# Kernel tuning notes

Hardware: AMD Instinct MI355X
Metric: run time of the kernel (lower is better)

## Reference

```python
import jax, jax.numpy as jnp
import numpy as np

V, E, H = 32000, 1024, 1024  # vocab, wemb, enc
T1, B = 129, 64


def setup_inputs() -> dict:
    key = jax.random.key(0)
    ks = jax.random.split(key, 6)
    sH = 1.0 / np.sqrt(H)
    data = jax.random.randint(ks[0], (T1, B), 0, V)
    mask = jnp.ones((T1, B), jnp.float32)
    emb = jax.random.normal(ks[1], (V, E), jnp.float32) * 0.02
    W_ih = jax.random.normal(ks[2], (E, 4 * H), jnp.float32) * sH
    W_hh = jax.random.normal(ks[3], (H, 4 * H), jnp.float32) * sH
    b = jnp.zeros((4 * H,), jnp.float32)
    Wr = jax.random.normal(ks[4], (E, H), jnp.float32) * sH  # readout: Linear(H -> E), torch weight (out,in)
    br = jnp.zeros((E,), jnp.float32)
    bd = jnp.zeros((V,), jnp.float32)  # decoder bias (weight tied to emb)
    return {"data": data, "mask": mask, "emb": emb, "W_ih": W_ih, "W_hh": W_hh,
            "b": b, "Wr": Wr, "br": br, "bd": bd}


def reference(data, mask, emb, W_ih, W_hh, b, Wr, br, bd):
    x_data = data[:-1]          # [Tx, B]
    y_data = data[1:]           # [Tx, B]
    m_all = mask[1:]            # note: source uses mask[1:] for BOTH x_mask and y_mask
    Tx, Bn = x_data.shape

    def step(carry, xs):
        ht, ct, loss = carry
        tx, ty, mt = xs                      # [B], [B], [B]
        x = emb[tx]                          # [B, E] embedding lookup
        g = x @ W_ih + ht @ W_hh + b         # [B, 4H]
        i, f, gg, o = jnp.split(g, 4, axis=1)
        i = jax.nn.sigmoid(i); f = jax.nn.sigmoid(f); o = jax.nn.sigmoid(o)
        gg = jnp.tanh(gg)
        cn = f * ct + i * gg
        hn = o * jnp.tanh(cn)
        mm = mt[:, None]
        ht2 = mm * hn + (1.0 - mm) * ht      # masked state update
        ct2 = mm * cn + (1.0 - mm) * ct
        out = ht2 @ Wr.T + br                # readout [B, E]
        logit = out @ emb.T + bd             # tied decoder [B, V]
        logp = jax.nn.log_softmax(logit, axis=1)
        nll = -jnp.take_along_axis(logp, ty[:, None], axis=1)[:, 0]
        loss = loss + jnp.mean(nll * mt)     # loss_reduction == 'org'
        return (ht2, ct2, loss), None

    init = (jnp.zeros((Bn, H), jnp.float32), jnp.zeros((Bn, H), jnp.float32),
            jnp.zeros((), jnp.float32))
    (_, _, loss), _ = jax.lax.scan(step, init, (x_data, y_data, m_all))
    return loss / Bn
```

## Files before the change

kernel.cpp:

```cpp
#include <hip/hip_runtime.h>
#include <stdint.h>

#define V_  32000
#define E_  1024
#define H_  1024
#define B_  64
#define T_  128
#define MROWS (T_ * B_)
#define NCB_ 250
#define NTG  32
#define ITEMS_PER_TG 258
#define TOTAL_ITEMS (NTG * ITEMS_PER_TG)

typedef __bf16 bf16x8 __attribute__((ext_vector_type(8)));
typedef float  f32x4  __attribute__((ext_vector_type(4)));

__device__ __forceinline__ uint16_t f2b(float f) {
  uint32_t u = __builtin_bit_cast(uint32_t, f);
  return (uint16_t)((u + 0x7fffu + ((u >> 16) & 1u)) >> 16);
}
__device__ __forceinline__ float b2f(uint16_t h) {
  uint32_t u = ((uint32_t)h) << 16;
  return __builtin_bit_cast(float, u);
}
__device__ __forceinline__ float fsig_(float x) {
  return __builtin_amdgcn_rcpf(1.0f + __expf(-x));
}
__device__ __forceinline__ float ftanh_(float x) {
  return 2.0f * __builtin_amdgcn_rcpf(1.0f + __expf(-2.0f * x)) - 1.0f;
}

__device__ __forceinline__ void gload16(const uint16_t* g, uint16_t* l) {
  __builtin_amdgcn_global_load_lds(
      (const __attribute__((address_space(1))) uint32_t*)g,
      (__attribute__((address_space(3))) uint32_t*)l,
      16, 0, 0);
}


__global__ void k_cvt(const float* __restrict__ src, uint16_t* __restrict__ dst, int n4) {
  int i = blockIdx.x * blockDim.x + threadIdx.x;
  int st = gridDim.x * blockDim.x;
  for (; i < n4; i += st) {
    float4 v = ((const float4*)src)[i];
    ushort4 o;
    o.x = f2b(v.x); o.y = f2b(v.y); o.z = f2b(v.z); o.w = f2b(v.w);
    ((ushort4*)dst)[i] = o;
  }
}

__global__ void k_tcvt(const float* __restrict__ src, uint16_t* __restrict__ dst,
                       int R, int C, int dstStride, int dstOff) {
  __shared__ float tile[32][33];
  int c0 = blockIdx.x * 32, r0 = blockIdx.y * 32;
  int tx = threadIdx.x, ty = threadIdx.y;
  for (int j = 0; j < 32; j += 8)
    tile[ty + j][tx] = src[(size_t)(r0 + ty + j) * C + c0 + tx];
  __syncthreads();
  for (int j = 0; j < 32; j += 8)
    dst[(size_t)(c0 + ty + j) * dstStride + dstOff + r0 + tx] = f2b(tile[tx][ty + j]);
}

__global__ void k_zero(uint4* p, int n) {
  int i = blockIdx.x * blockDim.x + threadIdx.x;
  int st = gridDim.x * blockDim.x;
  uint4 z = {0, 0, 0, 0};
  for (; i < n; i += st) p[i] = z;
}

__global__ __launch_bounds__(256) void k_xw(
    const int* __restrict__ data, const uint16_t* __restrict__ embB,
    const uint16_t* __restrict__ Wcat,
    const float* __restrict__ bias, uint16_t* __restrict__ xAll)
{
  __shared__ uint16_t lA[128 * 64];
  __shared__ uint16_t lB[128 * 64];

  int tid = threadIdx.x;
  int w = tid >> 6, l = tid & 63, lr = l & 15, lg = l >> 4;
  int wr = w >> 1, wc = w & 1;
  int m0 = blockIdx.x * 128;
  int n0 = blockIdx.y * 128;

  int stRow = l >> 3;
  int kswz  = ((l & 7) * 8) ^ ((stRow & 7) << 3);
  const uint16_t* aSrc[4];
  const uint16_t* bSrc[4];
#pragma unroll
  for (int cc = 0; cc < 4; ++cc) {
    int tok = data[m0 + w * 32 + cc * 8 + stRow];
    aSrc[cc] = embB + (size_t)tok * 1024 + kswz;
    bSrc[cc] = Wcat + (size_t)(n0 + w * 32 + cc * 8 + stRow) * 2048 + kswz;
  }

  f32x4 acc[4][4] = {};

  for (int kt = 0; kt < 1024; kt += 64) {
#pragma unroll
    for (int cc = 0; cc < 4; ++cc) {
      gload16(aSrc[cc] + kt, &lA[(w * 4 + cc) * 512]);
      gload16(bSrc[cc] + kt, &lB[(w * 4 + cc) * 512]);
    }
    __syncthreads();
#pragma unroll
    for (int ksub = 0; ksub < 2; ++ksub) {
      bf16x8 af[4], bfr[4];
      int ke = ksub * 32 + lg * 8;
#pragma unroll
      for (int mi = 0; mi < 4; ++mi) {
        int row = wr * 64 + mi * 16 + lr;
        af[mi] = *(const bf16x8*)&lA[row * 64 + (ke ^ ((row & 7) << 3))];
      }
#pragma unroll
      for (int ni = 0; ni < 4; ++ni) {
        int row = wc * 64 + ni * 16 + lr;
        bfr[ni] = *(const bf16x8*)&lB[row * 64 + (ke ^ ((row & 7) << 3))];
      }
#pragma unroll
      for (int mi = 0; mi < 4; ++mi)
#pragma unroll
        for (int ni = 0; ni < 4; ++ni)
          acc[mi][ni] = __builtin_amdgcn_mfma_f32_16x16x32_bf16(af[mi], bfr[ni], acc[mi][ni], 0, 0, 0);
    }
    __syncthreads();
  }

  float bv[4];
#pragma unroll
  for (int ni = 0; ni < 4; ++ni) bv[ni] = bias[n0 + wc * 64 + ni * 16 + lr];
#pragma unroll
  for (int mi = 0; mi < 4; ++mi)
#pragma unroll
    for (int ni = 0; ni < 4; ++ni) {
      int row = wr * 64 + mi * 16 + lg * 4;
      int col = n0 + wc * 64 + ni * 16 + lr;
#pragma unroll
      for (int r = 0; r < 4; ++r)
        xAll[(size_t)(m0 + row + r) * 4096 + col] = f2b(acc[mi][ni][r] + bv[ni]);
    }
}

__global__ __launch_bounds__(512) void k_mega(
    const uint16_t* __restrict__ xAll, const uint16_t* __restrict__ Wcat,
    const float* __restrict__ mask, uint16_t* __restrict__ hAll,
    uint32_t* __restrict__ flags,
    const uint16_t* __restrict__ embB, const uint16_t* __restrict__ WrB,
    const float* __restrict__ br, const float* __restrict__ bd,
    uint16_t* __restrict__ outAll, float2* __restrict__ part,
    uint32_t* __restrict__ projDone, uint32_t* __restrict__ workCtr)
{
  __shared__ alignas(16) char smem[151552];

  int tid = threadIdx.x;
  int blk = blockIdx.x;
  int w = tid >> 6, l = tid & 63, lr = l & 15, lg = l >> 4;

  if (blk < 64) {
    uint16_t* wh    = (uint16_t*)smem;
    uint16_t* xs0   = (uint16_t*)(smem + 131072);
    uint16_t* xs1   = (uint16_t*)(smem + 139264);
    uint16_t* hp0   = (uint16_t*)(smem + 147456);
    uint16_t* hp1   = (uint16_t*)(smem + 149504);
    uint16_t* xsb[2] = {xs0, xs1};
    uint16_t* hpb[2] = {hp0, hp1};

    int u0 = blk * 16;

    for (int it = 0; it < 16; ++it) {
      int ch = it * 512 + tid;
      int c  = ch >> 7;
      int kb = (ch & 127) * 16;
      int gRow = (c & 3) * 1024 + u0 + (c >> 2);
      uint4 v = *(const uint4*)((const char*)Wcat + (size_t)gRow * 4096 + 2048 + kb);
      *(uint4*)((char*)wh + c * 2048 + (kb ^ ((c & 7) << 4))) = v;
    }

    int wm = w >> 1, wn = w & 1;
    int q = lr & 3;

    const char* wb0 = (const char*)wh + (size_t)(wn * 32 + lr) * 2048;
    const char* wb1 = (const char*)wh + (size_t)(wn * 32 + 16 + lr) * 2048;
    int xr = (lr & 7) << 4;

    int sRow = tid >> 3, sQ = (tid >> 1) & 3, sHalf = tid & 1;
    const uint16_t* xSrc = xAll + (size_t)sRow * 4096 + sQ * 1024 + u0 + sHalf * 8;
    int xDstOff = sRow * 64 + sQ * 16 + sHalf * 8;
    int xoBase = (wm * 16 + lg * 4) * 64 + q * 16 + wn * 8 + (lr >> 2);

    float cR[2][4] = {}, hR[2][4] = {};

    *(uint4*)&xsb[0][xDstOff] = *(const uint4*)xSrc;
    __syncthreads();

    int cur = 0;
    for (int t = 0; t < T_; ++t) {
      float xwv[2][4], mm_[4];
#pragma unroll
      for (int ni = 0; ni < 2; ++ni)
#pragma unroll
        for (int r = 0; r < 4; ++r)
          xwv[ni][r] = b2f(xsb[cur][xoBase + r * 64 + ni * 4]);
#pragma unroll
      for (int r = 0; r < 4; ++r)
        mm_[r] = mask[(t + 1) * B_ + wm * 16 + lg * 4 + r];

      if (t + 1 < T_)
        *(uint4*)&xsb[cur ^ 1][xDstOff] = *(const uint4*)(xSrc + (size_t)(t + 1) * B_ * 4096);

      if (t > 0) {
        uint32_t tv = (uint32_t)t;
        while (!__all((int)(__hip_atomic_load(&flags[l], __ATOMIC_RELAXED,
                                              __HIP_MEMORY_SCOPE_AGENT) >= tv)))
          __builtin_amdgcn_s_sleep(1);
        asm volatile("" ::: "memory");
      }

      const uint16_t* aH = hAll + (size_t)t * (B_ * H_) + (size_t)(wm * 16 + lr) * H_ + lg * 8;

      f32x4 acc0 = {0.f, 0.f, 0.f, 0.f}, acc1 = {0.f, 0.f, 0.f, 0.f};
#pragma unroll 8
      for (int ks = 0; ks < 32; ++ks) {
        bf16x8 a = *(const bf16x8*)(aH + ks * 32);
        int ko = (ks * 64 + lg * 16) ^ xr;
        bf16x8 b0 = *(const bf16x8*)(wb0 + ko);
        bf16x8 b1 = *(const bf16x8*)(wb1 + ko);
        acc0 = __builtin_amdgcn_mfma_f32_16x16x32_bf16(a, b0, acc0, 0, 0, 0);
        acc1 = __builtin_amdgcn_mfma_f32_16x16x32_bf16(a, b1, acc1, 0, 0, 0);
      }

#pragma unroll
      for (int ni = 0; ni < 2; ++ni) {
        f32x4 accv = ni ? acc1 : acc0;
#pragma unroll
        for (int r = 0; r < 4; ++r) {
          float v0 = accv[r] + xwv[ni][r];
          float v1 = __shfl_xor(v0, 1, 64);
          float v2 = __shfl_xor(v0, 2, 64);
          float v3 = __shfl_xor(v0, 3, 64);
          float gi = (q == 0) ? v0 : (q == 1) ? v1 : (q == 2) ? v2 : v3;
          float gf = (q == 1) ? v0 : (q == 0) ? v1 : (q == 3) ? v2 : v3;
          float gg = (q == 2) ? v0 : (q == 3) ? v1 : (q == 0) ? v2 : v3;
          float go = (q == 3) ? v0 : (q == 2) ? v1 : (q == 1) ? v2 : v3;
          gi = fsig_(gi); gf = fsig_(gf); gg = ftanh_(gg); go = fsig_(go);
          float cn = gf * cR[ni][r] + gi * gg;
          float hn = go * ftanh_(cn);
          float mm = mm_[r];
          cR[ni][r] = mm * cn + (1.f - mm) * cR[ni][r];
          hR[ni][r] = mm * hn + (1.f - mm) * hR[ni][r];
          if (q == 0)
            hpb[cur][(wm * 16 + lg * 4 + r) * 16 + wn * 8 + ni * 4 + (lr >> 2)] = f2b(hR[ni][r]);
        }
      }

      __syncthreads();

      if (w == 0) {
        const unsigned long long* hp = (const unsigned long long*)hpb[cur];
        unsigned long long* hd =
            (unsigned long long*)(hAll + (size_t)(t + 1) * (B_ * H_) + (size_t)l * H_ + u0);
#pragma unroll
        for (int j = 0; j < 4; ++j)
          __hip_atomic_store(hd + j, hp[l * 4 + j],
                             __ATOMIC_RELAXED, __HIP_MEMORY_SCOPE_AGENT);
        asm volatile("s_waitcnt vmcnt(0)" ::: "memory");
        if (l == 0)
          __hip_atomic_store(&flags[blk], (uint32_t)(t + 1),
                             __ATOMIC_RELAXED, __HIP_MEMORY_SCOPE_AGENT);
      }
      cur ^= 1;
    }
  } else {
    uint16_t* lA  = (uint16_t*)smem;
    uint16_t* lB  = (uint16_t*)(smem + 32768);
    float2*   cm  = (float2*)(smem + 49152);
    uint32_t* sId = (uint32_t*)(smem + 53248);

    int stRow = l >> 3;
    int kswz  = ((l & 7) * 8) ^ ((stRow & 7) << 3);
    int wr = w >> 1;
    int wc = w & 1;

    for (;;) {
      __syncthreads();
      if (tid == 0)
        *sId = __hip_atomic_fetch_add(workCtr, 1u, __ATOMIC_RELAXED, __HIP_MEMORY_SCOPE_AGENT);
      __syncthreads();
      uint32_t id = *sId;
      if (id >= TOTAL_ITEMS) break;
      int tg = (int)(id / ITEMS_PER_TG), sub = (int)(id % ITEMS_PER_TG);
      int t0 = tg * 4;
      bool isProj = (sub < 8);

      const uint16_t* Abase;
      const uint16_t* Bbase;
      const float* biasp;
      if (isProj) {
        uint32_t tv = (uint32_t)(t0 + 4);
        while (!__all((int)(__hip_atomic_load(&flags[l], __ATOMIC_RELAXED,
                                              __HIP_MEMORY_SCOPE_AGENT) >= tv)))
          __builtin_amdgcn_s_sleep(4);
        asm volatile("" ::: "memory");
        Abase = hAll + (size_t)(t0 + 1) * (B_ * H_);
        Bbase = WrB + (size_t)(sub * 128) * 1024;
        biasp = br + sub * 128;
      } else {
        while (__hip_atomic_load(&projDone[tg], __ATOMIC_RELAXED,
                                 __HIP_MEMORY_SCOPE_AGENT) < 8u)
          __builtin_amdgcn_s_sleep(4);
        asm volatile("" ::: "memory");
        Abase = outAll + (size_t)t0 * B_ * 1024;
        Bbase = embB + (size_t)(sub - 8) * 128 * 1024;
        biasp = bd + (sub - 8) * 128;
      }

      const uint16_t* aS = Abase + (size_t)(w * 32 + stRow) * 1024 + kswz;
      const uint16_t* bS = Bbase + (size_t)(w * 16 + stRow) * 1024 + kswz;

      f32x4 acc[4][4] = {};
      for (int kt = 0; kt < 1024; kt += 64) {
#pragma unroll
        for (int cc = 0; cc < 4; ++cc)
          gload16(aS + (size_t)cc * 8 * 1024 + kt, &lA[(w * 4 + cc) * 512]);
#pragma unroll
        for (int cc = 0; cc < 2; ++cc)
          gload16(bS + (size_t)cc * 8 * 1024 + kt, &lB[(w * 2 + cc) * 512]);
        __syncthreads();
#pragma unroll
        for (int ksub = 0; ksub < 2; ++ksub) {
          int ke = ksub * 32 + lg * 8;
          bf16x8 af[4], bfr[4];
#pragma unroll
          for (int mi = 0; mi < 4; ++mi) {
            int row = wr * 64 + mi * 16 + lr;
            af[mi] = *(const bf16x8*)&lA[row * 64 + (ke ^ ((row & 7) << 3))];
          }
#pragma unroll
          for (int ni = 0; ni < 4; ++ni) {
            int row = wc * 64 + ni * 16 + lr;
            bfr[ni] = *(const bf16x8*)&lB[row * 64 + (ke ^ ((row & 7) << 3))];
          }
#pragma unroll
          for (int mi = 0; mi < 4; ++mi)
#pragma unroll
            for (int ni = 0; ni < 4; ++ni)
              acc[mi][ni] = __builtin_amdgcn_mfma_f32_16x16x32_bf16(af[mi], bfr[ni], acc[mi][ni], 0, 0, 0);
        }
        __syncthreads();
      }

      float bv[4];
#pragma unroll
      for (int ni = 0; ni < 4; ++ni) bv[ni] = biasp[wc * 64 + ni * 16 + lr];

      if (isProj) {
        int e0 = sub * 128;
        uint16_t* opack = lA;
#pragma unroll
        for (int chunk = 0; chunk < 4; ++chunk) {
          if (wr == chunk) {
#pragma unroll
            for (int mi = 0; mi < 4; ++mi)
#pragma unroll
              for (int ni = 0; ni < 4; ++ni)
#pragma unroll
                for (int r = 0; r < 4; ++r)
                  opack[(mi * 16 + lg * 4 + r) * 128 + wc * 64 + ni * 16 + lr]
                    = f2b(acc[mi][ni][r] + bv[ni]);
          }
          __syncthreads();
          const unsigned long long* op = (const unsigned long long*)opack;
#pragma unroll
          for (int j = 0; j < 4; ++j) {
            int g = j * 512 + tid;
            int row = g >> 5, seg = g & 31;
            unsigned long long* od =
                (unsigned long long*)(outAll + ((size_t)(t0 + chunk) * B_ + row) * 1024 + e0) + seg;
            __hip_atomic_store(od, op[g], __ATOMIC_RELAXED, __HIP_MEMORY_SCOPE_AGENT);
          }
          __syncthreads();
        }
        asm volatile("s_waitcnt vmcnt(0)" ::: "memory");
        __syncthreads();
        if (tid == 0)
          __hip_atomic_fetch_add(&projDone[tg], 1u, __ATOMIC_RELAXED, __HIP_MEMORY_SCOPE_AGENT);
      } else {
        int nc = sub - 8;
#pragma unroll
        for (int mi = 0; mi < 4; ++mi) {
#pragma unroll
          for (int r = 0; r < 4; ++r) {
            float mx = -1e30f;
#pragma unroll
            for (int ni = 0; ni < 4; ++ni) { acc[mi][ni][r] += bv[ni]; mx = fmaxf(mx, acc[mi][ni][r]); }
#pragma unroll
            for (int d = 1; d < 16; d <<= 1) mx = fmaxf(mx, __shfl_xor(mx, d, 64));
            float s = 0.f;
#pragma unroll
            for (int ni = 0; ni < 4; ++ni) s += expf(acc[mi][ni][r] - mx);
#pragma unroll
            for (int d = 1; d < 16; d <<= 1) s += __shfl_xor(s, d, 64);
            if (lr == 0) cm[wc * 256 + wr * 64 + mi * 16 + lg * 4 + r] = make_float2(mx, s);
          }
        }
        __syncthreads();
        if (tid < 256) {
          float2 p0 = cm[tid], p1 = cm[256 + tid];
          float M = fmaxf(p0.x, p1.x);
          float S = p0.y * expf(p0.x - M) + p1.y * expf(p1.x - M);
          part[(size_t)nc * MROWS + (size_t)t0 * B_ + tid] = make_float2(M, S);
        }
      }
    }
  }
}

__global__ __launch_bounds__(256) void k_tgt(
    const uint16_t* __restrict__ outAll, const uint16_t* __restrict__ embB,
    const float* __restrict__ bd, const int* __restrict__ data, float* __restrict__ tgt)
{
  int w = threadIdx.x >> 6, l = threadIdx.x & 63;
  int row = blockIdx.x * 4 + w;
  int t = row >> 6, b = row & 63;
  int ty = data[(t + 1) * B_ + b];
  const uint16_t* a = outAll + (size_t)row * E_;
  const uint16_t* e = embB + (size_t)ty * E_;
  float s = 0.f;
#pragma unroll
  for (int i0 = 0; i0 < 2; ++i0) {
    int i = (l + i0 * 64) * 8;
    bf16x8 av = *(const bf16x8*)(a + i);
    bf16x8 ev = *(const bf16x8*)(e + i);
#pragma unroll
    for (int j = 0; j < 8; ++j) s += (float)av[j] * (float)ev[j];
  }
#pragma unroll
  for (int d = 1; d < 64; d <<= 1) s += __shfl_xor(s, d, 64);
  if (l == 0) tgt[row] = s + bd[ty];
}

__global__ __launch_bounds__(256) void k_lse(
    const float2* __restrict__ part, const float* __restrict__ tgt,
    const float* __restrict__ mask, float* __restrict__ rowNll)
{
  int w = threadIdx.x >> 6, l = threadIdx.x & 63;
  int row = blockIdx.x * 4 + w;
  float m = -1e30f, s = 0.f;
  for (int cc = l; cc < NCB_; cc += 64) {
    float2 v = part[(size_t)cc * MROWS + row];
    float M = fmaxf(m, v.x);
    s = s * expf(m - M) + v.y * expf(v.x - M);
    m = M;
  }
#pragma unroll
  for (int d = 1; d < 64; d <<= 1) {
    float om = __shfl_xor(m, d, 64);
    float os = __shfl_xor(s, d, 64);
    float M = fmaxf(m, om);
    s = s * expf(m - M) + os * expf(om - M);
    m = M;
  }
  if (l == 0) {
    int t = row >> 6, b = row & 63;
    float nll = (m + logf(s)) - tgt[row];
    rowNll[row] = nll * mask[(t + 1) * B_ + b];
  }
}

__global__ void k_final2(const float* __restrict__ rowNll, float* __restrict__ out) {
  __shared__ float red[256];
  float s = 0.f;
  for (int i = threadIdx.x; i < MROWS; i += 256) s += rowNll[i];
  red[threadIdx.x] = s;
  __syncthreads();
  for (int st = 128; st > 0; st >>= 1) {
    if ((int)threadIdx.x < st) red[threadIdx.x] += red[threadIdx.x + st];
    __syncthreads();
  }
  if (threadIdx.x == 0) out[0] = red[0] / (float)(B_ * B_);
}

extern "C" void kernel_launch(void* const* d_in, const int* in_sizes, int n_in,
                              void* d_out, int out_size, void* d_ws, size_t ws_size,
                              hipStream_t stream)
{
  const int*   data = (const int*)  d_in[0];
  const float* mask = (const float*)d_in[1];
  const float* emb  = (const float*)d_in[2];
  const float* W_ih = (const float*)d_in[3];
  const float* W_hh = (const float*)d_in[4];
  const float* bias = (const float*)d_in[5];
  const float* Wr   = (const float*)d_in[6];
  const float* br   = (const float*)d_in[7];
  const float* bd   = (const float*)d_in[8];
  (void)in_sizes; (void)n_in; (void)out_size; (void)ws_size;

  char* ws = (char*)d_ws;
  size_t off = 0;
  auto alloc = [&](size_t bytes) -> char* {
    char* p = ws + off;
    off += (bytes + 255) & ~(size_t)255;
    return p;
  };
  uint16_t* embB   = (uint16_t*)alloc((size_t)V_ * E_ * 2);
  uint16_t* Wcat   = (uint16_t*)alloc((size_t)4 * H_ * 2048 * 2);
  uint16_t* WrB    = (uint16_t*)alloc((size_t)E_ * H_ * 2);
  uint16_t* hAll   = (uint16_t*)alloc((size_t)(T_ + 1) * B_ * H_ * 2);
  uint16_t* xAll   = (uint16_t*)alloc((size_t)MROWS * 4096 * 2);
  uint16_t* outAll = (uint16_t*)alloc((size_t)MROWS * E_ * 2);
  float2*   part   = (float2*)  alloc((size_t)NCB_ * MROWS * 8);
  float*    tgt    = (float*)   alloc((size_t)MROWS * 4);
  float*    rowNll = (float*)   alloc((size_t)MROWS * 4);
  uint32_t* syncb  = (uint32_t*)alloc(4096);
  uint32_t* flags    = syncb;
  uint32_t* projDone = syncb + 128;
  uint32_t* workCtr  = syncb + 512;

  k_cvt <<<2048, 256, 0, stream>>>(emb, embB, V_ * E_ / 4);
  k_cvt <<<256,  256, 0, stream>>>(Wr, WrB, E_ * H_ / 4);
  k_tcvt<<<dim3(4 * H_ / 32, E_ / 32), dim3(32, 8), 0, stream>>>(W_ih, Wcat, E_, 4 * H_, 2048, 0);
  k_tcvt<<<dim3(4 * H_ / 32, H_ / 32), dim3(32, 8), 0, stream>>>(W_hh, Wcat, H_, 4 * H_, 2048, 1024);
  k_zero<<<32, 256, 0, stream>>>((uint4*)hAll, B_ * H_ * 2 / 16);
  k_zero<<<1, 256, 0, stream>>>((uint4*)syncb, 4096 / 16);

  k_xw<<<dim3(MROWS / 128, 4096 / 128), 256, 0, stream>>>(data, embB, Wcat, bias, xAll);

  k_mega<<<256, 512, 0, stream>>>(xAll, Wcat, mask, hAll, flags,
                                  embB, WrB, br, bd, outAll, part,
                                  projDone, workCtr);

  k_tgt   <<<MROWS / 4, 256, 0, stream>>>(outAll, embB, bd, data, tgt);
  k_lse   <<<MROWS / 4, 256, 0, stream>>>(part, tgt, mask, rowNll);
  k_final2<<<1, 256, 0, stream>>>(rowNll, (float*)d_out);
}
```

Before: 2.128 ms.

## Split recurrent step wait into per-chunk flag waits and prefetch x-projection two steps ahead

The recurrent LSTM loop no longer waits for every producer flag before starting the h@W_hh matmul. It ballots the flags and waits only for the 16-lane group covering each K chunk, processing chunks in a block-rotated order so the MFMAs on ready chunks overlap with waiting on the rest. The x-projection input is now prefetched into a register two steps ahead instead of being loaded synchronously one step ahead. Consumer-side spin sleeps in the projection/decoder workers are lengthened to reduce polling pressure. The risk is extra ballot overhead and loop control on the critical serial path.

```diff
diff --git a/kernel.cpp b/kernel.cpp
--- a/kernel.cpp
+++ b/kernel.cpp
@@ -186,14 +186,20 @@
     const uint16_t* xSrc = xAll + (size_t)sRow * 4096 + sQ * 1024 + u0 + sHalf * 8;
     int xDstOff = sRow * 64 + sQ * 16 + sHalf * 8;
     int xoBase = (wm * 16 + lg * 4) * 64 + q * 16 + wn * 8 + (lr >> 2);
+    int rot = (blk >> 4) & 3;
 
     float cR[2][4] = {}, hR[2][4] = {};
 
-    *(uint4*)&xsb[0][xDstOff] = *(const uint4*)xSrc;
+    uint4 xwReg = *(const uint4*)xSrc;
+    *(uint4*)&xsb[0][xDstOff] = xwReg;
+    xwReg = *(const uint4*)(xSrc + (size_t)1 * B_ * 4096);
     __syncthreads();
 
     int cur = 0;
     for (int t = 0; t < T_; ++t) {
+      if (t + 1 < T_) *(uint4*)&xsb[cur ^ 1][xDstOff] = xwReg;
+      if (t + 2 < T_) xwReg = *(const uint4*)(xSrc + (size_t)(t + 2) * B_ * 4096);
+
       float xwv[2][4], mm_[4];
 #pragma unroll
       for (int ni = 0; ni < 2; ++ni)
@@ -204,28 +210,35 @@
       for (int r = 0; r < 4; ++r)
         mm_[r] = mask[(t + 1) * B_ + wm * 16 + lg * 4 + r];
 
-      if (t + 1 < T_)
-        *(uint4*)&xsb[cur ^ 1][xDstOff] = *(const uint4*)(xSrc + (size_t)(t + 1) * B_ * 4096);
-
+      const uint16_t* aH = hAll + (size_t)t * (B_ * H_) + (size_t)(wm * 16 + lr) * H_ + lg * 8;
+
+      f32x4 acc0 = {0.f, 0.f, 0.f, 0.f}, acc1 = {0.f, 0.f, 0.f, 0.f};
+      unsigned long long bal = 0;
       if (t > 0) {
-        uint32_t tv = (uint32_t)t;
-        while (!__all((int)(__hip_atomic_load(&flags[l], __ATOMIC_RELAXED,
-                                              __HIP_MEMORY_SCOPE_AGENT) >= tv)))
-          __builtin_amdgcn_s_sleep(1);
-        asm volatile("" ::: "memory");
-      }
-
-      const uint16_t* aH = hAll + (size_t)t * (B_ * H_) + (size_t)(wm * 16 + lr) * H_ + lg * 8;
-
-      f32x4 acc0 = {0.f, 0.f, 0.f, 0.f}, acc1 = {0.f, 0.f, 0.f, 0.f};
-#pragma unroll 8
-      for (int ks = 0; ks < 32; ++ks) {
-        bf16x8 a = *(const bf16x8*)(aH + ks * 32);
-        int ko = (ks * 64 + lg * 16) ^ xr;
-        bf16x8 b0 = *(const bf16x8*)(wb0 + ko);
-        bf16x8 b1 = *(const bf16x8*)(wb1 + ko);
-        acc0 = __builtin_amdgcn_mfma_f32_16x16x32_bf16(a, b0, acc0, 0, 0, 0);
-        acc1 = __builtin_amdgcn_mfma_f32_16x16x32_bf16(a, b1, acc1, 0, 0, 0);
+        uint32_t f = __hip_atomic_load(&flags[l], __ATOMIC_RELAXED, __HIP_MEMORY_SCOPE_AGENT);
+        bal = __ballot((int)(f >= (uint32_t)t));
+      }
+      for (int cc = 0; cc < 4; ++cc) {
+        int ch = (cc + rot) & 3;
+        if (t > 0) {
+          unsigned long long need = 0xFFFFull << (ch * 16);
+          while ((bal & need) != need) {
+            __builtin_amdgcn_s_sleep(1);
+            uint32_t f = __hip_atomic_load(&flags[l], __ATOMIC_RELAXED, __HIP_MEMORY_SCOPE_AGENT);
+            bal = __ballot((int)(f >= (uint32_t)t));
+          }
+          asm volatile("" ::: "memory");
+        }
+#pragma unroll
+        for (int k2 = 0; k2 < 8; ++k2) {
+          int ks = ch * 8 + k2;
+          bf16x8 a = *(const bf16x8*)(aH + ks * 32);
+          int ko = (ks * 64 + lg * 16) ^ xr;
+          bf16x8 b0 = *(const bf16x8*)(wb0 + ko);
+          bf16x8 b1 = *(const bf16x8*)(wb1 + ko);
+          acc0 = __builtin_amdgcn_mfma_f32_16x16x32_bf16(a, b0, acc0, 0, 0, 0);
+          acc1 = __builtin_amdgcn_mfma_f32_16x16x32_bf16(a, b1, acc1, 0, 0, 0);
+        }
       }
 
 #pragma unroll
@@ -298,7 +311,7 @@
         uint32_t tv = (uint32_t)(t0 + 4);
         while (!__all((int)(__hip_atomic_load(&flags[l], __ATOMIC_RELAXED,
                                               __HIP_MEMORY_SCOPE_AGENT) >= tv)))
-          __builtin_amdgcn_s_sleep(4);
+          __builtin_amdgcn_s_sleep(8);
         asm volatile("" ::: "memory");
         Abase = hAll + (size_t)(t0 + 1) * (B_ * H_);
         Bbase = WrB + (size_t)(sub * 128) * 1024;
@@ -306,7 +319,7 @@
       } else {
         while (__hip_atomic_load(&projDone[tg], __ATOMIC_RELAXED,
                                  __HIP_MEMORY_SCOPE_AGENT) < 8u)
-          __builtin_amdgcn_s_sleep(4);
+          __builtin_amdgcn_s_sleep(8);
         asm volatile("" ::: "memory");
         Abase = outAll + (size_t)t0 * B_ * 1024;
         Bbase = embB + (size_t)(sub - 8) * 128 * 1024;
```

Result: slower. 2.187 ms (+2.8%).
